# Kernel optimization log

Hardware: AMD Instinct MI355X
Metric: run time of the kernel (lower is better)

## Reference

```python
import jax, jax.numpy as jnp
import numpy as np

TEMPERATURE = 1.0
EPS = 1e-8

def setup_inputs() -> dict:
    key = jax.random.key(0)
    k1, k2, k3 = jax.random.split(key, 3)
    B, A, D = 1024, 64, 1024
    q_embeddings = jax.random.normal(k1, (B, D), dtype=jnp.float32)
    a_list_embeddings = jax.random.normal(k2, (B, A, D), dtype=jnp.float32)
    a_list_scores = jax.random.uniform(k3, (B, A), dtype=jnp.float32)
    return {"q_embeddings": q_embeddings,
            "a_list_embeddings": a_list_embeddings,
            "a_list_scores": a_list_scores}

def _dcg(order, scores):
    # order: [B, A] indices (descending sort), scores: [B, A]
    A = scores.shape[-1]
    ranks = jnp.arange(1, A + 1, dtype=scores.dtype)  # [A]
    gain = jnp.take_along_axis(scores, order, axis=-1)  # [B, A]
    return jnp.sum(gain / jnp.log2(ranks + 1.0), axis=-1)  # [B]

def reference(q_embeddings, a_list_embeddings, a_list_scores):
    # sim[b, a] = q[b] . answers[b, a] / T
    sim = jnp.einsum('bd,bad->ba', q_embeddings, a_list_embeddings) / TEMPERATURE
    sim_probs = jax.nn.softmax(sim, axis=-1)                       # [B, A]
    target_probs = jax.nn.softmax(a_list_scores / TEMPERATURE, -1)  # [B, A]
    log_pred = jnp.log(sim_probs + EPS)
    # KL(target || pred) with reduction='sum' per sample
    kl = jnp.sum(target_probs * (jnp.log(target_probs) - log_pred), axis=-1)  # [B]
    loss = jnp.mean(kl)
    # NDCG metric
    pred_order = jnp.argsort(-sim, axis=-1)
    ideal_order = jnp.argsort(-a_list_scores, axis=-1)
    pred_dcg = _dcg(pred_order, a_list_scores)
    ideal_dcg = _dcg(ideal_order, a_list_scores)
    avg_ndcg = jnp.mean(pred_dcg / (ideal_dcg + EPS))
    return loss, avg_ndcg
```

## Files before the change

kernel.cpp:

```cpp
#include <hip/hip_runtime.h>
#include <math.h>

constexpr int B = 1024;
constexpr int A = 64;
constexpr int D = 1024;
constexpr float EPS = 1e-8f;

__device__ __forceinline__ float wave_reduce_sum(float v) {
    #pragma unroll
    for (int off = 32; off > 0; off >>= 1) v += __shfl_xor(v, off, 64);
    return v;
}
__device__ __forceinline__ float wave_reduce_max(float v) {
    #pragma unroll
    for (int off = 32; off > 0; off >>= 1) v = fmaxf(v, __shfl_xor(v, off, 64));
    return v;
}

__global__ __launch_bounds__(256) void rank_main(
    const float* __restrict__ q,
    const float* __restrict__ emb,
    const float* __restrict__ scores,
    float* __restrict__ ws)
{
    const int b    = blockIdx.x;
    const int tid  = threadIdx.x;
    const int wave = tid >> 6;
    const int lane = tid & 63;

    __shared__ float sim_s[A];

    const float4* q4 = reinterpret_cast<const float4*>(q + (size_t)b * D);
    const float4 qv0 = q4[lane];
    const float4 qv1 = q4[lane + 64];
    const float4 qv2 = q4[lane + 128];
    const float4 qv3 = q4[lane + 192];

    const int a0 = wave * 16;
    #pragma unroll 4
    for (int ai = 0; ai < 16; ++ai) {
        const int a = a0 + ai;
        const float4* e4 = reinterpret_cast<const float4*>(
            emb + ((size_t)b * A + a) * D);
        const float4 e0 = e4[lane];
        const float4 e1 = e4[lane + 64];
        const float4 e2 = e4[lane + 128];
        const float4 e3 = e4[lane + 192];
        float acc = qv0.x*e0.x + qv0.y*e0.y + qv0.z*e0.z + qv0.w*e0.w
                  + qv1.x*e1.x + qv1.y*e1.y + qv1.z*e1.z + qv1.w*e1.w
                  + qv2.x*e2.x + qv2.y*e2.y + qv2.z*e2.z + qv2.w*e2.w
                  + qv3.x*e3.x + qv3.y*e3.y + qv3.z*e3.z + qv3.w*e3.w;
        acc = wave_reduce_sum(acc);
        if (lane == 0) sim_s[a] = acc;
    }
    __syncthreads();

    if (tid >= 64) return;

    const int a = lane;
    const float s  = sim_s[a];
    const float sc = scores[(size_t)b * A + a];

    const float m  = wave_reduce_max(s);
    const float ex = expf(s - m);
    const float se = wave_reduce_sum(ex);
    const float p  = ex / se;
    const float logp = logf(p + EPS);

    const float tm = wave_reduce_max(sc);
    const float te = expf(sc - tm);
    const float ts = wave_reduce_sum(te);
    const float t  = te / ts;
    const float logt = logf(t);

    const float kl = wave_reduce_sum(t * (logt - logp));

    int rp = 1, ri = 1;
    #pragma unroll
    for (int r = 0; r < 64; ++r) {
        const float so = __shfl(s,  r, 64);
        const float co = __shfl(sc, r, 64);
        rp += (so > s)  || (so == s  && r < a);
        ri += (co > sc) || (co == sc && r < a);
    }

    const float pd = wave_reduce_sum(sc / log2f((float)(rp + 1)));
    const float id = wave_reduce_sum(sc / log2f((float)(ri + 1)));

    if (lane == 0) {
        ws[b]     = kl;
        ws[B + b] = pd / (id + EPS);
    }
}

__global__ __launch_bounds__(256) void rank_final(
    const float* __restrict__ ws, float* __restrict__ out)
{
    const int tid  = threadIdx.x;
    const int wave = tid >> 6;
    const int lane = tid & 63;
    __shared__ float sk[4], sn[4];

    float kl = 0.f, nd = 0.f;
    for (int i = tid; i < B; i += 256) {
        kl += ws[i];
        nd += ws[B + i];
    }
    kl = wave_reduce_sum(kl);
    nd = wave_reduce_sum(nd);
    if (lane == 0) { sk[wave] = kl; sn[wave] = nd; }
    __syncthreads();
    if (tid == 0) {
        const float K = sk[0] + sk[1] + sk[2] + sk[3];
        const float N = sn[0] + sn[1] + sn[2] + sn[3];
        out[0] = K * (1.0f / B);
        out[1] = N * (1.0f / B);
    }
}

extern "C" void kernel_launch(void* const* d_in, const int* in_sizes, int n_in,
                              void* d_out, int out_size, void* d_ws, size_t ws_size,
                              hipStream_t stream) {
    const float* q      = (const float*)d_in[0];
    const float* emb    = (const float*)d_in[1];
    const float* scores = (const float*)d_in[2];
    float* out = (float*)d_out;
    float* ws  = (float*)d_ws;

    rank_main<<<B, 256, 0, stream>>>(q, emb, scores, ws);
    rank_final<<<1, 256, 0, stream>>>(ws, out);
}
```

Before: 369.7 us.

## Split similarity and loss into separate kernels with finer block granularity

Splits the fused kernel into a similarity kernel that uses two blocks per batch row (8 answers per wave) and a loss/NDCG kernel that processes four rows per block, one per wave. The goal is more parallelism and memory-level concurrency in the bandwidth-heavy dot products, and no idle waves during the per-row softmax and ranking phase. The cost is an extra kernel launch and writing and re-reading the similarity matrix through global memory. It also adds an occupancy hint and splits the dot-product accumulation into partial sums.

```diff
diff --git a/kernel.cpp b/kernel.cpp
--- a/kernel.cpp
+++ b/kernel.cpp
@@ -17,18 +17,16 @@
     return v;
 }
 
-__global__ __launch_bounds__(256) void rank_main(
+__global__ __launch_bounds__(256, 6) void sim_kernel(
     const float* __restrict__ q,
     const float* __restrict__ emb,
-    const float* __restrict__ scores,
-    float* __restrict__ ws)
+    float* __restrict__ sims)
 {
-    const int b    = blockIdx.x;
+    const int b    = blockIdx.x >> 1;
+    const int h    = blockIdx.x & 1;
     const int tid  = threadIdx.x;
     const int wave = tid >> 6;
     const int lane = tid & 63;
-
-    __shared__ float sim_s[A];
 
     const float4* q4 = reinterpret_cast<const float4*>(q + (size_t)b * D);
     const float4 qv0 = q4[lane];
@@ -36,9 +34,9 @@
     const float4 qv2 = q4[lane + 128];
     const float4 qv3 = q4[lane + 192];
 
-    const int a0 = wave * 16;
-    #pragma unroll 4
-    for (int ai = 0; ai < 16; ++ai) {
+    const int a0 = h * 32 + wave * 8;
+    #pragma unroll 2
+    for (int ai = 0; ai < 8; ++ai) {
         const int a = a0 + ai;
         const float4* e4 = reinterpret_cast<const float4*>(
             emb + ((size_t)b * A + a) * D);
@@ -46,20 +44,30 @@
         const float4 e1 = e4[lane + 64];
         const float4 e2 = e4[lane + 128];
         const float4 e3 = e4[lane + 192];
-        float acc = qv0.x*e0.x + qv0.y*e0.y + qv0.z*e0.z + qv0.w*e0.w
-                  + qv1.x*e1.x + qv1.y*e1.y + qv1.z*e1.z + qv1.w*e1.w
-                  + qv2.x*e2.x + qv2.y*e2.y + qv2.z*e2.z + qv2.w*e2.w
-                  + qv3.x*e3.x + qv3.y*e3.y + qv3.z*e3.z + qv3.w*e3.w;
+        float s0 = qv0.x*e0.x + qv0.y*e0.y + qv0.z*e0.z + qv0.w*e0.w;
+        float s1 = qv1.x*e1.x + qv1.y*e1.y + qv1.z*e1.z + qv1.w*e1.w;
+        float s2 = qv2.x*e2.x + qv2.y*e2.y + qv2.z*e2.z + qv2.w*e2.w;
+        float s3 = qv3.x*e3.x + qv3.y*e3.y + qv3.z*e3.z + qv3.w*e3.w;
+        float acc = (s0 + s1) + (s2 + s3);
         acc = wave_reduce_sum(acc);
-        if (lane == 0) sim_s[a] = acc;
+        if (lane == 0) sims[(size_t)b * A + a] = acc;
     }
-    __syncthreads();
+}
 
-    if (tid >= 64) return;
+__global__ __launch_bounds__(256) void loss_kernel(
+    const float* __restrict__ sims,
+    const float* __restrict__ scores,
+    float* __restrict__ kl_out,
+    float* __restrict__ nd_out)
+{
+    const int tid  = threadIdx.x;
+    const int wave = tid >> 6;
+    const int lane = tid & 63;
+    const int r    = blockIdx.x * 4 + wave;
 
     const int a = lane;
-    const float s  = sim_s[a];
-    const float sc = scores[(size_t)b * A + a];
+    const float s  = sims[(size_t)r * A + a];
+    const float sc = scores[(size_t)r * A + a];
 
     const float m  = wave_reduce_max(s);
     const float ex = expf(s - m);
@@ -77,24 +85,25 @@
 
     int rp = 1, ri = 1;
     #pragma unroll
-    for (int r = 0; r < 64; ++r) {
-        const float so = __shfl(s,  r, 64);
-        const float co = __shfl(sc, r, 64);
-        rp += (so > s)  || (so == s  && r < a);
-        ri += (co > sc) || (co == sc && r < a);
+    for (int o = 0; o < 64; ++o) {
+        const float so = __shfl(s,  o, 64);
+        const float co = __shfl(sc, o, 64);
+        rp += (so > s)  || (so == s  && o < a);
+        ri += (co > sc) || (co == sc && o < a);
     }
 
     const float pd = wave_reduce_sum(sc / log2f((float)(rp + 1)));
     const float id = wave_reduce_sum(sc / log2f((float)(ri + 1)));
 
     if (lane == 0) {
-        ws[b]     = kl;
-        ws[B + b] = pd / (id + EPS);
+        kl_out[r] = kl;
+        nd_out[r] = pd / (id + EPS);
     }
 }
 
-__global__ __launch_bounds__(256) void rank_final(
-    const float* __restrict__ ws, float* __restrict__ out)
+__global__ __launch_bounds__(256) void final_kernel(
+    const float* __restrict__ kl_in, const float* __restrict__ nd_in,
+    float* __restrict__ out)
 {
     const int tid  = threadIdx.x;
     const int wave = tid >> 6;
@@ -103,18 +112,16 @@
 
     float kl = 0.f, nd = 0.f;
     for (int i = tid; i < B; i += 256) {
-        kl += ws[i];
-        nd += ws[B + i];
+        kl += kl_in[i];
+        nd += nd_in[i];
     }
     kl = wave_reduce_sum(kl);
     nd = wave_reduce_sum(nd);
     if (lane == 0) { sk[wave] = kl; sn[wave] = nd; }
     __syncthreads();
     if (tid == 0) {
-        const float K = sk[0] + sk[1] + sk[2] + sk[3];
-        const float N = sn[0] + sn[1] + sn[2] + sn[3];
-        out[0] = K * (1.0f / B);
-        out[1] = N * (1.0f / B);
+        out[0] = (sk[0] + sk[1] + sk[2] + sk[3]) * (1.0f / B);
+        out[1] = (sn[0] + sn[1] + sn[2] + sn[3]) * (1.0f / B);
     }
 }
 
@@ -125,8 +132,12 @@
     const float* emb    = (const float*)d_in[1];
     const float* scores = (const float*)d_in[2];
     float* out = (float*)d_out;
-    float* ws  = (float*)d_ws;
 
-    rank_main<<<B, 256, 0, stream>>>(q, emb, scores, ws);
-    rank_final<<<1, 256, 0, stream>>>(ws, out);
+    float* sims = (float*)d_ws;
+    float* kl_b = sims + (size_t)B * A;
+    float* nd_b = kl_b + B;
+
+    sim_kernel  <<<2 * B, 256, 0, stream>>>(q, emb, sims);
+    loss_kernel <<<B / 4, 256, 0, stream>>>(sims, scores, kl_b, nd_b);
+    final_kernel<<<1,     256, 0, stream>>>(kl_b, nd_b, out);
 }
```

Result: no change. 368.7 us (-0.3%).
